# Kernel tuning notes

Measured on AMD Instinct MI355X. Metric: run time of the kernel, lower is better.

The kernel has to match this reference:

```python
import jax, jax.numpy as jnp
import numpy as np

TOPK_RADIUS = 1   # get_radius(topk=1): nearest non-self neighbor distance
TOPK_NEIGH = 10   # torch.topk(weights, 10)


def _soft_instance_loss(z_i, z_j, z_i_prob, z_j_prob, pseudo_label):
    n = z_i.shape[0]
    invalid = pseudo_label == -1
    same = pseudo_label[:, None] == pseudo_label[None, :]          # [n, n]
    same = same & (~invalid)[:, None] & (~invalid)[None, :]
    same = same & (~jnp.eye(n, dtype=bool))                        # remove diagonal
    mask = jnp.tile(same.astype(z_i_prob.dtype), (2, 2))           # [2n, 2n]

    feats = jnp.concatenate([z_i, z_j], axis=0)                    # [2n, d]
    probs = jnp.concatenate([z_i_prob, z_j_prob], axis=0)          # [2n, C]

    # ---- no_grad block of soft_neighbors_loss_L2 ----
    f = jax.lax.stop_gradient(feats)
    sq = jnp.sum(f * f, axis=1)
    d2 = sq[:, None] + sq[None, :] - 2.0 * (f @ f.T)
    pd = jnp.sqrt(jnp.maximum(d2, 0.0))                            # torch.cdist, [2n, 2n]
    b = 2 * n
    radius = jnp.sort(pd, axis=1)[:, TOPK_RADIUS][:, None]         # per-row 1-NN radius
    w = 1.0 - jnp.clip((pd - radius) / radius, 0.0, 1.0) - jnp.eye(b, dtype=pd.dtype)
    top, idx = jax.lax.top_k(w, TOPK_NEIGH)                        # [2n, 10]
    weights = jnp.zeros((b, b), pd.dtype).at[jnp.arange(b)[:, None], idx].set(top)
    weights = jax.lax.stop_gradient(weights)
    # ---- end no_grad ----

    inner = probs @ probs.T                                        # [2n, 2n]
    pull = weights * inner                                         # boosting=True -> pull only
    return jnp.mean(pull * mask)


def setup_inputs() -> dict:
    key = jax.random.key(0)
    k1, k2, k3, k4, k5 = jax.random.split(key, 5)
    n, d, C = 2048, 512, 128
    z_i = jax.random.normal(k1, (n, d), dtype=jnp.float32)
    z_j = jax.random.normal(k2, (n, d), dtype=jnp.float32)
    z_i_prob = jax.nn.softmax(jax.random.normal(k3, (n, C), dtype=jnp.float32), axis=-1)
    z_j_prob = jax.nn.softmax(jax.random.normal(k4, (n, C), dtype=jnp.float32), axis=-1)
    pseudo_label = jax.random.randint(k5, (n,), 0, C, dtype=jnp.int64 if jax.config.jax_enable_x64 else jnp.int32)
    return {"z_i": z_i, "z_j": z_j, "z_i_prob": z_i_prob, "z_j_prob": z_j_prob, "pseudo_label": pseudo_label}


def reference(z_i, z_j, z_i_prob, z_j_prob, pseudo_label):
    return _soft_instance_loss(z_i, z_j, z_i_prob, z_j_prob, pseudo_label)
```

## Files before the change

### kernel.cpp

```cpp
#include <hip/hip_runtime.h>
#include <hip/hip_bf16.h>
#include <hip/hip_fp16.h>
#include <cstdint>
#include <cstddef>

typedef __attribute__((ext_vector_type(8))) short short8;
typedef __attribute__((ext_vector_type(8))) unsigned short ushort8;
typedef __attribute__((ext_vector_type(4))) float f32x4;

#define BM 128
#define BN 128
#define BK 64
#define NSEL 10

__device__ __forceinline__ void gload_lds16(const void* g, void* l) {
  typedef const __attribute__((address_space(1))) void* gp_t;
  typedef __attribute__((address_space(3))) void* lp_t;
  __builtin_amdgcn_global_load_lds((gp_t)(unsigned long long)(uintptr_t)g,
                                   (lp_t)(unsigned int)(unsigned long long)(uintptr_t)l,
                                   16, 0, 0);
}

__device__ __forceinline__ unsigned short f2h_bits(float f) {
  __half h = __float2half(f);
  return *reinterpret_cast<unsigned short*>(&h);
}

__device__ __forceinline__ float h2f_bits(unsigned short us) {
  __half h = *reinterpret_cast<__half*>(&us);
  return __half2float(h);
}

__global__ __launch_bounds__(256)
void prep_kernel(const float* __restrict__ zi, const float* __restrict__ zj,
                 unsigned short* __restrict__ fb, float* __restrict__ sq,
                 int n, int d) {
  __shared__ float wred[4];
  const int row = blockIdx.x;
  const int t = threadIdx.x, lane = t & 63, wave = t >> 6;
  const float* src = (row < n) ? (zi + (size_t)row * d) : (zj + (size_t)(row - n) * d);
  float s = 0.f;
  for (int c = t; c < d; c += 256) {
    float v = src[c];
    s += v * v;
    __hip_bfloat16 h = __float2bfloat16(v);
    fb[(size_t)row * d + c] = *reinterpret_cast<const unsigned short*>(&h);
  }
#pragma unroll
  for (int o = 32; o; o >>= 1) s += __shfl_xor(s, o, 64);
  if (lane == 0) wred[wave] = s;
  __syncthreads();
  if (t == 0) sq[row] = ((wred[0] + wred[1]) + wred[2]) + wred[3];
}

__global__ __launch_bounds__(256)
void gemm_pd_kernel(const unsigned short* __restrict__ fb,
                    const float* __restrict__ sq,
                    __half* __restrict__ pdh, int b, int d) {
  __shared__ unsigned long long smem64[4096];
  unsigned short* smA = (unsigned short*)smem64;
  unsigned short* smB = smA + 8192;
  const int t = threadIdx.x;
  const int lane = t & 63;
  const int wave = t >> 6;
  const int wr = wave >> 1, wc = wave & 1;
  const int rowBase = blockIdx.y * BM;
  const int colBase = blockIdx.x * BN;
  const int l15 = lane & 15, l4 = lane >> 4;
  const int rsw = l15 & 7;

  f32x4 acc[4][4] = {};

  for (int kt = 0; kt < d; kt += BK) {
#pragma unroll
    for (int it = 0; it < 4; ++it) {
      const int c = it * 256 + t;
      const int r = c >> 3;
      const int us = (c & 7) ^ (r & 7);
      gload_lds16(fb + (size_t)(rowBase + r) * d + kt + us * 8, (char*)smA + c * 16);
      gload_lds16(fb + (size_t)(colBase + r) * d + kt + us * 8, (char*)smB + c * 16);
    }
    __syncthreads();
#pragma unroll
    for (int ks = 0; ks < 2; ++ks) {
      short8 af[4], bfr[4];
#pragma unroll
      for (int m = 0; m < 4; ++m)
        af[m] = *(const short8*)&smA[(wr * 64 + m * 16 + l15) * BK + (((ks * 4 + l4) ^ rsw) * 8)];
#pragma unroll
      for (int nn = 0; nn < 4; ++nn)
        bfr[nn] = *(const short8*)&smB[(wc * 64 + nn * 16 + l15) * BK + (((ks * 4 + l4) ^ rsw) * 8)];
#pragma unroll
      for (int m = 0; m < 4; ++m)
#pragma unroll
        for (int nn = 0; nn < 4; ++nn)
          acc[m][nn] = __builtin_amdgcn_mfma_f32_16x16x32_bf16(af[m], bfr[nn], acc[m][nn], 0, 0, 0);
    }
    __syncthreads();
  }

  unsigned short* tileC = (unsigned short*)smem64;
#pragma unroll
  for (int m = 0; m < 4; ++m) {
    const int r0l = wr * 64 + m * 16 + l4 * 4;
    const int gr0 = rowBase + r0l;
    const float sqr0 = sq[gr0], sqr1 = sq[gr0 + 1], sqr2 = sq[gr0 + 2], sqr3 = sq[gr0 + 3];
#pragma unroll
    for (int nn = 0; nn < 4; ++nn) {
      const int cl = wc * 64 + nn * 16 + l15;
      const int gc = colBase + cl;
      const float sqc = sq[gc];
      float d20 = fmaxf(sqr0 + sqc - 2.0f * acc[m][nn][0], 0.0f);
      float d21 = fmaxf(sqr1 + sqc - 2.0f * acc[m][nn][1], 0.0f);
      float d22 = fmaxf(sqr2 + sqc - 2.0f * acc[m][nn][2], 0.0f);
      float d23 = fmaxf(sqr3 + sqc - 2.0f * acc[m][nn][3], 0.0f);
      unsigned short b0 = (gr0 == gc) ? (unsigned short)0x7C00 : f2h_bits(d20);
      unsigned short b1 = (gr0 + 1 == gc) ? (unsigned short)0x7C00 : f2h_bits(d21);
      unsigned short b2 = (gr0 + 2 == gc) ? (unsigned short)0x7C00 : f2h_bits(d22);
      unsigned short b3 = (gr0 + 3 == gc) ? (unsigned short)0x7C00 : f2h_bits(d23);
#pragma unroll
      for (int rg = 0; rg < 4; ++rg) {
        const int rl = r0l + rg;
        const int dw = rl * 64 + (cl >> 1);
        const int phys = dw ^ (((rl >> 2) & 3) << 3);
        unsigned short bits = (rg == 0) ? b0 : (rg == 1) ? b1 : (rg == 2) ? b2 : b3;
        tileC[phys * 2 + (cl & 1)] = bits;
      }
    }
  }
  __syncthreads();

#pragma unroll
  for (int it2 = 0; it2 < 16; ++it2) {
    const int rl = it2 * 8 + (t >> 5);
    const int dwb = rl * 64 + (t & 31) * 2;
    const int phys = dwb ^ (((rl >> 2) & 3) << 3);
    const unsigned long long v = *(const unsigned long long*)((const char*)smem64 + (size_t)phys * 4);
    *(unsigned long long*)((char*)pdh + ((size_t)(rowBase + rl) * b + colBase + (t & 31) * 4) * 2) = v;
  }
}

__global__ __launch_bounds__(256, 2)
void topk_loss_kernel(const __half* __restrict__ pdh,
                      const float* __restrict__ pi, const float* __restrict__ pj,
                      const int* __restrict__ labels,
                      float* __restrict__ rowsum,
                      int n, int C, int b) {
  const int t = threadIdx.x, lane = t & 63, wave = t >> 6;
  const int row = blockIdx.x * 4 + wave;

  const ushort8* rowp = (const ushort8*)(pdh + (size_t)row * b);
  unsigned vv[8][8];
  unsigned cmin[8];
#pragma unroll
  for (int ch = 0; ch < 8; ++ch) {
    ushort8 h = rowp[ch * 64 + lane];
    unsigned mn = 0xFFFFFFFFu;
#pragma unroll
    for (int j = 0; j < 8; ++j) {
      unsigned pk = ((unsigned)h[j] << 16) | (unsigned)(ch * 512 + lane * 8 + j);
      vv[ch][j] = pk;
      mn = min(mn, pk);
    }
    cmin[ch] = mn;
  }

  unsigned key[NSEL];
#pragma unroll
  for (int r = 0; r < NSEL; ++r) {
    unsigned best = cmin[0];
#pragma unroll
    for (int ch = 1; ch < 8; ++ch) best = min(best, cmin[ch]);
#pragma unroll
    for (int o = 32; o; o >>= 1) {
      unsigned q = __shfl_xor(best, o, 64);
      best = min(best, q);
    }
    key[r] = best;
    const int idx = (int)(best & 0xFFFFu);
    if (((idx >> 3) & 63) == lane) {
      const int ch = idx >> 9, jj = idx & 7;
#pragma unroll
      for (int cc = 0; cc < 8; ++cc) {
        if (cc == ch) {
          unsigned mn = 0xFFFFFFFFu;
#pragma unroll
          for (int j = 0; j < 8; ++j) {
            if (j == jj) vv[cc][j] = 0xFFFFFFFFu;
            mn = min(mn, vv[cc][j]);
          }
          cmin[cc] = mn;
        }
      }
    }
  }

  const float r0 = sqrtf(h2f_bits((unsigned short)(key[0] >> 16)));
  const float inv_r0 = 1.0f / r0;
  const int ri = (row < n) ? row : row - n;
  const int li = labels[ri];
  const float* pme = (row < n) ? (pi + (size_t)row * C) : (pj + (size_t)(row - n) * C);
  const float pr0 = pme[lane], pr1 = pme[lane + 64];

  float tot = 0.f;
#pragma unroll
  for (int k = 0; k < NSEL; ++k) {
    const int j = (int)(key[k] & 0xFFFFu);
    const int rj = (j < n) ? j : j - n;
    const int lj = labels[rj];
    const bool m = (li != -1) & (lj != -1) & (li == lj) & (ri != rj);
    if (m) {
      const float* q = (j < n) ? (pi + (size_t)j * C) : (pj + (size_t)(j - n) * C);
      float part = pr0 * q[lane] + pr1 * q[lane + 64];
#pragma unroll
      for (int o = 32; o; o >>= 1) part += __shfl_xor(part, o, 64);
      const float pd = sqrtf(h2f_bits((unsigned short)(key[k] >> 16)));
      const float w = 1.0f - fminf(fmaxf((pd - r0) * inv_r0, 0.0f), 1.0f);
      tot += w * part;
    }
  }
  if (lane == 0) rowsum[row] = tot;
}

__global__ __launch_bounds__(256)
void final_reduce_kernel(const float* __restrict__ rowsum, float* __restrict__ out, int b) {
  __shared__ float wredf[4];
  const int t = threadIdx.x, lane = t & 63, wave = t >> 6;
  float s = 0.f;
  for (int c = t; c < b; c += 256) s += rowsum[c];
#pragma unroll
  for (int o = 32; o; o >>= 1) s += __shfl_xor(s, o, 64);
  if (lane == 0) wredf[wave] = s;
  __syncthreads();
  if (t == 0) {
    float tot = ((wredf[0] + wredf[1]) + wredf[2]) + wredf[3];
    out[0] = tot / ((float)b * (float)b);
  }
}

extern "C" void kernel_launch(void* const* d_in, const int* in_sizes, int n_in,
                              void* d_out, int out_size, void* d_ws, size_t ws_size,
                              hipStream_t stream) {
  const float* zi = (const float*)d_in[0];
  const float* zj = (const float*)d_in[1];
  const float* pi = (const float*)d_in[2];
  const float* pj = (const float*)d_in[3];
  const int* labels = (const int*)d_in[4];

  const int n = in_sizes[4];
  const int d = in_sizes[0] / n;
  const int C = in_sizes[2] / n;
  const int b = 2 * n;

  char* ws = (char*)d_ws;
  size_t off = 0;
  unsigned short* fb = (unsigned short*)(ws + off);
  off += ((size_t)b * d * 2 + 255) & ~(size_t)255;
  float* sq = (float*)(ws + off);
  off += ((size_t)b * 4 + 255) & ~(size_t)255;
  float* rowsum = (float*)(ws + off);
  off += ((size_t)b * 4 + 255) & ~(size_t)255;
  __half* pdh = (__half*)(ws + off);
  off += (size_t)b * b * 2;
  if (ws_size < off) return;

  prep_kernel<<<b, 256, 0, stream>>>(zi, zj, fb, sq, n, d);
  dim3 grid(b / BN, b / BM);
  gemm_pd_kernel<<<grid, 256, 0, stream>>>(fb, sq, pdh, b, d);
  topk_loss_kernel<<<b / 4, 256, 0, stream>>>(pdh, pi, pj, labels, rowsum, n, C, b);
  final_reduce_kernel<<<1, 256, 0, stream>>>(rowsum, (float*)d_out, b);
}
```

Baseline: 56.02 us.

## Enlarge GEMM tile to 256x256 with 8 waves and double-buffered LDS prefetch

```diff
diff --git a/kernel.cpp b/kernel.cpp
--- a/kernel.cpp
+++ b/kernel.cpp
@@ -8,9 +8,6 @@
 typedef __attribute__((ext_vector_type(8))) unsigned short ushort8;
 typedef __attribute__((ext_vector_type(4))) float f32x4;
 
-#define BM 128
-#define BN 128
-#define BK 64
 #define NSEL 10
 
 __device__ __forceinline__ void gload_lds16(const void* g, void* l) {
@@ -53,61 +50,85 @@
   if (t == 0) sq[row] = ((wred[0] + wred[1]) + wred[2]) + wred[3];
 }
 
-__global__ __launch_bounds__(256)
+__global__ __launch_bounds__(512)
 void gemm_pd_kernel(const unsigned short* __restrict__ fb,
                     const float* __restrict__ sq,
                     __half* __restrict__ pdh, int b, int d) {
-  __shared__ unsigned long long smem64[4096];
-  unsigned short* smA = (unsigned short*)smem64;
-  unsigned short* smB = smA + 8192;
+  __shared__ char smem[131072];
   const int t = threadIdx.x;
   const int lane = t & 63;
   const int wave = t >> 6;
-  const int wr = wave >> 1, wc = wave & 1;
-  const int rowBase = blockIdx.y * BM;
-  const int colBase = blockIdx.x * BN;
+  const int wm = wave >> 2, wn = wave & 3;
+  const int rowBase = blockIdx.y * 256;
+  const int colBase = blockIdx.x * 256;
   const int l15 = lane & 15, l4 = lane >> 4;
   const int rsw = l15 & 7;
-
-  f32x4 acc[4][4] = {};
-
-  for (int kt = 0; kt < d; kt += BK) {
-#pragma unroll
-    for (int it = 0; it < 4; ++it) {
-      const int c = it * 256 + t;
-      const int r = c >> 3;
-      const int us = (c & 7) ^ (r & 7);
-      gload_lds16(fb + (size_t)(rowBase + r) * d + kt + us * 8, (char*)smA + c * 16);
-      gload_lds16(fb + (size_t)(colBase + r) * d + kt + us * 8, (char*)smB + c * 16);
-    }
-    __syncthreads();
+  const int nt = d >> 6;
+
+  f32x4 acc[8][4] = {};
+
+  auto stage_tile = [&](int bufOff, int kt) {
+#pragma unroll
+    for (int half = 0; half < 2; ++half) {
+#pragma unroll
+      for (int ab = 0; ab < 2; ++ab) {
+#pragma unroll
+        for (int i = 0; i < 2; ++i) {
+          const int c = half * 1024 + i * 512 + t;
+          const int r = c >> 3;
+          const int us = (c & 7) ^ (r & 7);
+          const int gbase = (ab == 0) ? rowBase : colBase;
+          gload_lds16(fb + (size_t)(gbase + r) * d + kt * 64 + us * 8,
+                      smem + bufOff + ab * 32768 + c * 16);
+        }
+      }
+    }
+  };
+
+  int curOff = 0;
+  stage_tile(0, 0);
+
+  for (int kt = 0; kt < nt; ++kt) {
+    if (kt + 1 < nt) {
+      stage_tile(curOff ^ 65536, kt + 1);
+      asm volatile("s_waitcnt vmcnt(8)" ::: "memory");
+    } else {
+      asm volatile("s_waitcnt vmcnt(0)" ::: "memory");
+    }
+    __builtin_amdgcn_s_barrier();
+    __builtin_amdgcn_sched_barrier(0);
+
+    const unsigned short* smA = (const unsigned short*)(smem + curOff);
+    const unsigned short* smB = (const unsigned short*)(smem + curOff + 32768);
 #pragma unroll
     for (int ks = 0; ks < 2; ++ks) {
-      short8 af[4], bfr[4];
-#pragma unroll
-      for (int m = 0; m < 4; ++m)
-        af[m] = *(const short8*)&smA[(wr * 64 + m * 16 + l15) * BK + (((ks * 4 + l4) ^ rsw) * 8)];
+      short8 bf[4];
 #pragma unroll
       for (int nn = 0; nn < 4; ++nn)
-        bfr[nn] = *(const short8*)&smB[(wc * 64 + nn * 16 + l15) * BK + (((ks * 4 + l4) ^ rsw) * 8)];
-#pragma unroll
-      for (int m = 0; m < 4; ++m)
+        bf[nn] = *(const short8*)&smB[(wn * 64 + nn * 16 + l15) * 64 + (((ks * 4 + l4) ^ rsw) * 8)];
+#pragma unroll
+      for (int m = 0; m < 8; ++m) {
+        short8 af = *(const short8*)&smA[(wm * 128 + m * 16 + l15) * 64 + (((ks * 4 + l4) ^ rsw) * 8)];
 #pragma unroll
         for (int nn = 0; nn < 4; ++nn)
-          acc[m][nn] = __builtin_amdgcn_mfma_f32_16x16x32_bf16(af[m], bfr[nn], acc[m][nn], 0, 0, 0);
-    }
-    __syncthreads();
-  }
-
-  unsigned short* tileC = (unsigned short*)smem64;
-#pragma unroll
-  for (int m = 0; m < 4; ++m) {
-    const int r0l = wr * 64 + m * 16 + l4 * 4;
+          acc[m][nn] = __builtin_amdgcn_mfma_f32_16x16x32_bf16(af, bf[nn], acc[m][nn], 0, 0, 0);
+      }
+    }
+    __builtin_amdgcn_sched_barrier(0);
+    __builtin_amdgcn_s_barrier();
+    __builtin_amdgcn_sched_barrier(0);
+    curOff ^= 65536;
+  }
+
+  unsigned short* tileC = (unsigned short*)smem;
+#pragma unroll
+  for (int m = 0; m < 8; ++m) {
+    const int r0l = wm * 128 + m * 16 + l4 * 4;
     const int gr0 = rowBase + r0l;
     const float sqr0 = sq[gr0], sqr1 = sq[gr0 + 1], sqr2 = sq[gr0 + 2], sqr3 = sq[gr0 + 3];
 #pragma unroll
     for (int nn = 0; nn < 4; ++nn) {
-      const int cl = wc * 64 + nn * 16 + l15;
+      const int cl = wn * 64 + nn * 16 + l15;
       const int gc = colBase + cl;
       const float sqc = sq[gc];
       float d20 = fmaxf(sqr0 + sqc - 2.0f * acc[m][nn][0], 0.0f);
@@ -121,7 +142,7 @@
 #pragma unroll
       for (int rg = 0; rg < 4; ++rg) {
         const int rl = r0l + rg;
-        const int dw = rl * 64 + (cl >> 1);
+        const int dw = rl * 128 + (cl >> 1);
         const int phys = dw ^ (((rl >> 2) & 3) << 3);
         unsigned short bits = (rg == 0) ? b0 : (rg == 1) ? b1 : (rg == 2) ? b2 : b3;
         tileC[phys * 2 + (cl & 1)] = bits;
@@ -131,12 +152,12 @@
   __syncthreads();
 
 #pragma unroll
-  for (int it2 = 0; it2 < 16; ++it2) {
-    const int rl = it2 * 8 + (t >> 5);
-    const int dwb = rl * 64 + (t & 31) * 2;
+  for (int it2 = 0; it2 < 32; ++it2) {
+    const int rl = it2 * 8 + (t >> 6);
+    const int dwb = rl * 128 + (t & 63) * 2;
     const int phys = dwb ^ (((rl >> 2) & 3) << 3);
-    const unsigned long long v = *(const unsigned long long*)((const char*)smem64 + (size_t)phys * 4);
-    *(unsigned long long*)((char*)pdh + ((size_t)(rowBase + rl) * b + colBase + (t & 31) * 4) * 2) = v;
+    const unsigned long long v = *(const unsigned long long*)((const char*)smem + (size_t)phys * 4);
+    *(unsigned long long*)((char*)pdh + ((size_t)(rowBase + rl) * b + colBase + (t & 63) * 4) * 2) = v;
   }
 }
 
@@ -265,8 +286,8 @@
   if (ws_size < off) return;
 
   prep_kernel<<<b, 256, 0, stream>>>(zi, zj, fb, sq, n, d);
-  dim3 grid(b / BN, b / BM);
-  gemm_pd_kernel<<<grid, 256, 0, stream>>>(fb, sq, pdh, b, d);
+  dim3 grid(b / 256, b / 256);
+  gemm_pd_kernel<<<grid, 512, 0, stream>>>(fb, sq, pdh, b, d);
   topk_loss_kernel<<<b / 4, 256, 0, stream>>>(pdh, pi, pj, labels, rowsum, n, C, b);
   final_reduce_kernel<<<1, 256, 0, stream>>>(rowsum, (float*)d_out, b);
 }
```

Result: faster. 52.53 us (-6.2%).
